# Performance work log

Hardware: AMD Instinct MI355X
Metric: run time of the kernel (lower is better)

## Reference

```python
import jax, jax.numpy as jnp
import numpy as np

# convert_dict = {0: 1, 1: 0, 2: -1}: maps argmax position -> signed label
CONVERT = jnp.array([1, 0, -1], dtype=jnp.int32)


def setup_inputs() -> dict:
    key = jax.random.key(0)
    N = 8388608  # rows; each row is [up(3), none(3), down(3)]
    inputs = jax.random.normal(key, (N, 9), dtype=jnp.float32)
    return {"inputs": inputs}


def reference(inputs):
    # [N, 9] -> [N, 3 groups (up, none, down), 3]
    x = inputs.reshape(-1, 3, 3)

    # __get_max_index: if the max is tied within a 3-vector -> 0,
    # else convert_dict[argmax] in {1, 0, -1}
    maxv = jnp.max(x, axis=-1, keepdims=True)
    ties = jnp.sum((x == maxv).astype(jnp.int32), axis=-1) > 1  # [N, 3]
    mi = jnp.where(ties, 0, CONVERT[jnp.argmax(x, axis=-1)])    # [N, 3] int32

    # calc_value = abs(max_index_none) * (up_idx + none_idx + down_idx)
    calc = jnp.abs(mi[:, 1]) * (mi[:, 0] + mi[:, 1] + mi[:, 2])  # [N] int32

    # __remove_ex_data: keep vector only when sign(calc) matches sign(max_index),
    # otherwise replace by zeros
    c = calc[:, None]
    keep = ((c > 0) & (mi > 0)) | ((c < 0) & (mi < 0)) | ((c == 0) & (mi == 0))
    vecs = jnp.where(keep[..., None], x, jnp.float32(0))  # [N, 3, 3]

    # __concat_result branch: calc==0 -> compare element 1; calc>=1 -> element 0;
    # calc<=-1 -> element 2 (calc is always an integer in {-3..3})
    idx = jnp.where(calc == 0, 1, jnp.where(calc >= 1, 0, 2))  # [N]

    # __find_best_data: argmax over [up[idx], none[idx], down[idx]] picks the
    # winning group (tf.argmax over the concat -> 0=up, 1=none, 2=down, which
    # matches group order here); return that whole (possibly zeroed) 3-vector
    vals = jnp.take_along_axis(vecs, idx[:, None, None], axis=2)[..., 0]  # [N, 3]
    win = jnp.argmax(vals, axis=1)  # [N]
    out = jnp.take_along_axis(vecs, win[:, None, None], axis=1)[:, 0, :]  # [N, 3]
    return out
```

## Files before the change

### kernel.cpp

```cpp
#include <hip/hip_runtime.h>

#define ROWS_PER_BLOCK 256
#define BLOCK_THREADS 256

__global__ __launch_bounds__(BLOCK_THREADS) void pick_rows_kernel(
    const float* __restrict__ in, float* __restrict__ out, long long nrows) {

    __shared__ float lds_in[ROWS_PER_BLOCK * 9];
    __shared__ float lds_out[ROWS_PER_BLOCK * 3];

    const int tid = threadIdx.x;
    const long long tileStride = (long long)gridDim.x * ROWS_PER_BLOCK;

    for (long long rowBase = (long long)blockIdx.x * ROWS_PER_BLOCK;
         rowBase < nrows; rowBase += tileStride) {

        const long long rowsLeft = nrows - rowBase;
        const int rowsHere = rowsLeft < ROWS_PER_BLOCK ? (int)rowsLeft : ROWS_PER_BLOCK;

        const float* src = in + rowBase * 9;
        if (rowsHere == ROWS_PER_BLOCK) {
            const float4* src4 = reinterpret_cast<const float4*>(src);
            #pragma unroll
            for (int i = 0; i < 576 / BLOCK_THREADS + 1; ++i) {
                int k = tid + i * BLOCK_THREADS;
                if (k < 576) {
                    float4 v = src4[k];
                    lds_in[k * 4 + 0] = v.x;
                    lds_in[k * 4 + 1] = v.y;
                    lds_in[k * 4 + 2] = v.z;
                    lds_in[k * 4 + 3] = v.w;
                }
            }
        } else {
            const int nf = rowsHere * 9;
            for (int k = tid; k < nf; k += BLOCK_THREADS) lds_in[k] = src[k];
        }
        __syncthreads();

        if (tid < rowsHere) {
            float v[3][3];
            #pragma unroll
            for (int j = 0; j < 3; ++j)
                #pragma unroll
                for (int k = 0; k < 3; ++k)
                    v[j][k] = lds_in[tid * 9 + j * 3 + k];

            int mi[3];
            #pragma unroll
            for (int j = 0; j < 3; ++j) {
                const float a = v[j][0], b = v[j][1], c = v[j][2];
                const float m = fmaxf(a, fmaxf(b, c));
                const int ties = (int)(a == m) + (int)(b == m) + (int)(c == m);
                int am;
                if (a == m) am = 0;
                else if (b == m) am = 1;
                else am = 2;
                mi[j] = (ties > 1) ? 0 : (1 - am);
            }

            const int calc = (mi[1] < 0 ? -mi[1] : mi[1]) * (mi[0] + mi[1] + mi[2]);

            bool keep[3];
            #pragma unroll
            for (int j = 0; j < 3; ++j)
                keep[j] = (calc > 0 && mi[j] > 0) ||
                          (calc < 0 && mi[j] < 0) ||
                          (calc == 0 && mi[j] == 0);

            const int idx = (calc == 0) ? 1 : ((calc >= 1) ? 0 : 2);

            float vals[3];
            #pragma unroll
            for (int j = 0; j < 3; ++j)
                vals[j] = keep[j] ? v[j][idx] : 0.0f;

            int win = 0;
            float best = vals[0];
            if (vals[1] > best) { best = vals[1]; win = 1; }
            if (vals[2] > best) { win = 2; }

            const bool kw = keep[win];
            #pragma unroll
            for (int k = 0; k < 3; ++k)
                lds_out[tid * 3 + k] = kw ? v[win][k] : 0.0f;
        }
        __syncthreads();

        float* dst = out + rowBase * 3;
        if (rowsHere == ROWS_PER_BLOCK) {
            float4* dst4 = reinterpret_cast<float4*>(dst);
            if (tid < 192) {
                float4 o;
                o.x = lds_out[tid * 4 + 0];
                o.y = lds_out[tid * 4 + 1];
                o.z = lds_out[tid * 4 + 2];
                o.w = lds_out[tid * 4 + 3];
                dst4[tid] = o;
            }
        } else {
            const int nf = rowsHere * 3;
            for (int k = tid; k < nf; k += BLOCK_THREADS) dst[k] = lds_out[k];
        }
        __syncthreads();
    }
}

extern "C" void kernel_launch(void* const* d_in, const int* in_sizes, int n_in,
                              void* d_out, int out_size, void* d_ws, size_t ws_size,
                              hipStream_t stream) {
    const float* in = (const float*)d_in[0];
    float* out = (float*)d_out;
    const long long nrows = (long long)in_sizes[0] / 9;

    const long long tiles = (nrows + ROWS_PER_BLOCK - 1) / ROWS_PER_BLOCK;
    int grid = (int)(tiles < 2048 ? tiles : 2048);
    pick_rows_kernel<<<grid, BLOCK_THREADS, 0, stream>>>(in, out, nrows);
}
```

Baseline: 80.53 us.

## Replace LDS-staged tiles with per-thread 4-row register loads

New measurement: 80.19 us. No clear change (-0.4%).

```diff
diff --git a/kernel.cpp b/kernel.cpp
--- a/kernel.cpp
+++ b/kernel.cpp
@@ -1,108 +1,109 @@
 #include <hip/hip_runtime.h>
 
-#define ROWS_PER_BLOCK 256
-#define BLOCK_THREADS 256
 
-__global__ __launch_bounds__(BLOCK_THREADS) void pick_rows_kernel(
+__device__ __forceinline__ void compute_row(
+    float v00, float v01, float v02,
+    float v10, float v11, float v12,
+    float v20, float v21, float v22,
+    float& o0, float& o1, float& o2) {
+
+    float v[3][3] = {{v00, v01, v02}, {v10, v11, v12}, {v20, v21, v22}};
+
+    int mi[3];
+#pragma unroll
+    for (int j = 0; j < 3; ++j) {
+        const float a = v[j][0], b = v[j][1], c = v[j][2];
+        const float m = fmaxf(a, fmaxf(b, c));
+        const int ties = (int)(a == m) + (int)(b == m) + (int)(c == m);
+        int am;
+        if (a == m) am = 0;
+        else if (b == m) am = 1;
+        else am = 2;
+        mi[j] = (ties > 1) ? 0 : (1 - am);
+    }
+
+    const int calc = (mi[1] < 0 ? -mi[1] : mi[1]) * (mi[0] + mi[1] + mi[2]);
+
+    bool keep[3];
+#pragma unroll
+    for (int j = 0; j < 3; ++j)
+        keep[j] = (calc > 0 && mi[j] > 0) ||
+                  (calc < 0 && mi[j] < 0) ||
+                  (calc == 0 && mi[j] == 0);
+
+    const int idx = (calc == 0) ? 1 : ((calc >= 1) ? 0 : 2);
+
+    float vals[3];
+#pragma unroll
+    for (int j = 0; j < 3; ++j) {
+        const float vj = (idx == 0) ? v[j][0] : ((idx == 2) ? v[j][2] : v[j][1]);
+        vals[j] = keep[j] ? vj : 0.0f;
+    }
+
+    const bool w1 = vals[1] > vals[0];
+    const float b01 = w1 ? vals[1] : vals[0];
+    const bool w2 = vals[2] > b01;
+
+    const bool keepw = w2 ? keep[2] : (w1 ? keep[1] : keep[0]);
+
+    const float r0 = w2 ? v[2][0] : (w1 ? v[1][0] : v[0][0]);
+    const float r1 = w2 ? v[2][1] : (w1 ? v[1][1] : v[0][1]);
+    const float r2 = w2 ? v[2][2] : (w1 ? v[1][2] : v[0][2]);
+
+    o0 = keepw ? r0 : 0.0f;
+    o1 = keepw ? r1 : 0.0f;
+    o2 = keepw ? r2 : 0.0f;
+}
+
+__global__ __launch_bounds__(256) void pick_rows_kernel(
     const float* __restrict__ in, float* __restrict__ out, long long nrows) {
 
-    __shared__ float lds_in[ROWS_PER_BLOCK * 9];
-    __shared__ float lds_out[ROWS_PER_BLOCK * 3];
+    const long long t = (long long)blockIdx.x * blockDim.x + threadIdx.x;
+    const long long r0 = t * 4;
+    if (r0 >= nrows) return;
 
-    const int tid = threadIdx.x;
-    const long long tileStride = (long long)gridDim.x * ROWS_PER_BLOCK;
+    if (r0 + 4 <= nrows) {
+        const float4* p4 = reinterpret_cast<const float4*>(in + r0 * 9);
+        float4 f[9];
+#pragma unroll
+        for (int i = 0; i < 9; ++i) f[i] = p4[i];
 
-    for (long long rowBase = (long long)blockIdx.x * ROWS_PER_BLOCK;
-         rowBase < nrows; rowBase += tileStride) {
+        float x[36];
+#pragma unroll
+        for (int i = 0; i < 9; ++i) {
+            x[i * 4 + 0] = f[i].x;
+            x[i * 4 + 1] = f[i].y;
+            x[i * 4 + 2] = f[i].z;
+            x[i * 4 + 3] = f[i].w;
+        }
 
-        const long long rowsLeft = nrows - rowBase;
-        const int rowsHere = rowsLeft < ROWS_PER_BLOCK ? (int)rowsLeft : ROWS_PER_BLOCK;
+        float o[12];
+#pragma unroll
+        for (int j = 0; j < 4; ++j) {
+            compute_row(x[j * 9 + 0], x[j * 9 + 1], x[j * 9 + 2],
+                        x[j * 9 + 3], x[j * 9 + 4], x[j * 9 + 5],
+                        x[j * 9 + 6], x[j * 9 + 7], x[j * 9 + 8],
+                        o[j * 3 + 0], o[j * 3 + 1], o[j * 3 + 2]);
+        }
 
-        const float* src = in + rowBase * 9;
-        if (rowsHere == ROWS_PER_BLOCK) {
-            const float4* src4 = reinterpret_cast<const float4*>(src);
-            #pragma unroll
-            for (int i = 0; i < 576 / BLOCK_THREADS + 1; ++i) {
-                int k = tid + i * BLOCK_THREADS;
-                if (k < 576) {
-                    float4 v = src4[k];
-                    lds_in[k * 4 + 0] = v.x;
-                    lds_in[k * 4 + 1] = v.y;
-                    lds_in[k * 4 + 2] = v.z;
-                    lds_in[k * 4 + 3] = v.w;
-                }
-            }
-        } else {
-            const int nf = rowsHere * 9;
-            for (int k = tid; k < nf; k += BLOCK_THREADS) lds_in[k] = src[k];
+        float4* q4 = reinterpret_cast<float4*>(out + r0 * 3);
+        float4 q;
+        q.x = o[0];  q.y = o[1];  q.z = o[2];  q.w = o[3];
+        q4[0] = q;
+        q.x = o[4];  q.y = o[5];  q.z = o[6];  q.w = o[7];
+        q4[1] = q;
+        q.x = o[8];  q.y = o[9];  q.z = o[10]; q.w = o[11];
+        q4[2] = q;
+    } else {
+        for (long long r = r0; r < nrows; ++r) {
+            const float* p = in + r * 9;
+            float o0, o1, o2;
+            compute_row(p[0], p[1], p[2], p[3], p[4], p[5], p[6], p[7], p[8],
+                        o0, o1, o2);
+            out[r * 3 + 0] = o0;
+            out[r * 3 + 1] = o1;
+            out[r * 3 + 2] = o2;
         }
-        __syncthreads();
-
-        if (tid < rowsHere) {
-            float v[3][3];
-            #pragma unroll
-            for (int j = 0; j < 3; ++j)
-                #pragma unroll
-                for (int k = 0; k < 3; ++k)
-                    v[j][k] = lds_in[tid * 9 + j * 3 + k];
-
-            int mi[3];
-            #pragma unroll
-            for (int j = 0; j < 3; ++j) {
-                const float a = v[j][0], b = v[j][1], c = v[j][2];
-                const float m = fmaxf(a, fmaxf(b, c));
-                const int ties = (int)(a == m) + (int)(b == m) + (int)(c == m);
-                int am;
-                if (a == m) am = 0;
-                else if (b == m) am = 1;
-                else am = 2;
-                mi[j] = (ties > 1) ? 0 : (1 - am);
-            }
-
-            const int calc = (mi[1] < 0 ? -mi[1] : mi[1]) * (mi[0] + mi[1] + mi[2]);
-
-            bool keep[3];
-            #pragma unroll
-            for (int j = 0; j < 3; ++j)
-                keep[j] = (calc > 0 && mi[j] > 0) ||
-                          (calc < 0 && mi[j] < 0) ||
-                          (calc == 0 && mi[j] == 0);
-
-            const int idx = (calc == 0) ? 1 : ((calc >= 1) ? 0 : 2);
-
-            float vals[3];
-            #pragma unroll
-            for (int j = 0; j < 3; ++j)
-                vals[j] = keep[j] ? v[j][idx] : 0.0f;
-
-            int win = 0;
-            float best = vals[0];
-            if (vals[1] > best) { best = vals[1]; win = 1; }
-            if (vals[2] > best) { win = 2; }
-
-            const bool kw = keep[win];
-            #pragma unroll
-            for (int k = 0; k < 3; ++k)
-                lds_out[tid * 3 + k] = kw ? v[win][k] : 0.0f;
-        }
-        __syncthreads();
-
-        float* dst = out + rowBase * 3;
-        if (rowsHere == ROWS_PER_BLOCK) {
-            float4* dst4 = reinterpret_cast<float4*>(dst);
-            if (tid < 192) {
-                float4 o;
-                o.x = lds_out[tid * 4 + 0];
-                o.y = lds_out[tid * 4 + 1];
-                o.z = lds_out[tid * 4 + 2];
-                o.w = lds_out[tid * 4 + 3];
-                dst4[tid] = o;
-            }
-        } else {
-            const int nf = rowsHere * 3;
-            for (int k = tid; k < nf; k += BLOCK_THREADS) dst[k] = lds_out[k];
-        }
-        __syncthreads();
     }
 }
 
@@ -113,7 +114,8 @@
     float* out = (float*)d_out;
     const long long nrows = (long long)in_sizes[0] / 9;
 
-    const long long tiles = (nrows + ROWS_PER_BLOCK - 1) / ROWS_PER_BLOCK;
-    int grid = (int)(tiles < 2048 ? tiles : 2048);
-    pick_rows_kernel<<<grid, BLOCK_THREADS, 0, stream>>>(in, out, nrows);
+    const long long nthreads = (nrows + 3) / 4;
+    const int block = 256;
+    const long long nblocks = (nthreads + block - 1) / block;
+    pick_rows_kernel<<<(int)nblocks, block, 0, stream>>>(in, out, nrows);
 }
```

## Use nontemporal loads, drop output LDS staging, and make row selection branchless

Applied to the files above, without the earlier changes.

New measurement: 70.26 us. -12.8%, faster.

```diff
diff --git a/kernel.cpp b/kernel.cpp
--- a/kernel.cpp
+++ b/kernel.cpp
@@ -1,13 +1,64 @@
 #include <hip/hip_runtime.h>
+
+typedef float floatx4 __attribute__((ext_vector_type(4)));
 
 #define ROWS_PER_BLOCK 256
 #define BLOCK_THREADS 256
+
+
+__device__ __forceinline__ void compute_row(
+    const float v[3][3], float& o0, float& o1, float& o2) {
+
+    int mi[3];
+#pragma unroll
+    for (int j = 0; j < 3; ++j) {
+        const float a = v[j][0], b = v[j][1], c = v[j][2];
+        const float m = fmaxf(a, fmaxf(b, c));
+        const int ties = (int)(a == m) + (int)(b == m) + (int)(c == m);
+        int am;
+        if (a == m) am = 0;
+        else if (b == m) am = 1;
+        else am = 2;
+        mi[j] = (ties > 1) ? 0 : (1 - am);
+    }
+
+    const int calc = (mi[1] < 0 ? -mi[1] : mi[1]) * (mi[0] + mi[1] + mi[2]);
+
+    bool keep[3];
+#pragma unroll
+    for (int j = 0; j < 3; ++j)
+        keep[j] = (calc > 0 && mi[j] > 0) ||
+                  (calc < 0 && mi[j] < 0) ||
+                  (calc == 0 && mi[j] == 0);
+
+    const int idx = (calc == 0) ? 1 : ((calc >= 1) ? 0 : 2);
+
+    float vals[3];
+#pragma unroll
+    for (int j = 0; j < 3; ++j) {
+        const float vj = (idx == 0) ? v[j][0] : ((idx == 2) ? v[j][2] : v[j][1]);
+        vals[j] = keep[j] ? vj : 0.0f;
+    }
+
+    const bool w1 = vals[1] > vals[0];
+    const float b01 = w1 ? vals[1] : vals[0];
+    const bool w2 = vals[2] > b01;
+
+    const bool keepw = w2 ? keep[2] : (w1 ? keep[1] : keep[0]);
+
+    const float r0 = w2 ? v[2][0] : (w1 ? v[1][0] : v[0][0]);
+    const float r1 = w2 ? v[2][1] : (w1 ? v[1][1] : v[0][1]);
+    const float r2 = w2 ? v[2][2] : (w1 ? v[1][2] : v[0][2]);
+
+    o0 = keepw ? r0 : 0.0f;
+    o1 = keepw ? r1 : 0.0f;
+    o2 = keepw ? r2 : 0.0f;
+}
 
 __global__ __launch_bounds__(BLOCK_THREADS) void pick_rows_kernel(
     const float* __restrict__ in, float* __restrict__ out, long long nrows) {
 
     __shared__ float lds_in[ROWS_PER_BLOCK * 9];
-    __shared__ float lds_out[ROWS_PER_BLOCK * 3];
 
     const int tid = threadIdx.x;
     const long long tileStride = (long long)gridDim.x * ROWS_PER_BLOCK;
@@ -18,21 +69,29 @@
         const long long rowsLeft = nrows - rowBase;
         const int rowsHere = rowsLeft < ROWS_PER_BLOCK ? (int)rowsLeft : ROWS_PER_BLOCK;
 
-        const float* src = in + rowBase * 9;
         if (rowsHere == ROWS_PER_BLOCK) {
-            const float4* src4 = reinterpret_cast<const float4*>(src);
-            #pragma unroll
-            for (int i = 0; i < 576 / BLOCK_THREADS + 1; ++i) {
-                int k = tid + i * BLOCK_THREADS;
-                if (k < 576) {
-                    float4 v = src4[k];
-                    lds_in[k * 4 + 0] = v.x;
-                    lds_in[k * 4 + 1] = v.y;
-                    lds_in[k * 4 + 2] = v.z;
-                    lds_in[k * 4 + 3] = v.w;
+            const floatx4* src4 = reinterpret_cast<const floatx4*>(in + rowBase * 9);
+            {
+                floatx4 v0 = __builtin_nontemporal_load(src4 + tid);
+                floatx4 v1 = __builtin_nontemporal_load(src4 + tid + 256);
+                lds_in[tid * 4 + 0] = v0.x;
+                lds_in[tid * 4 + 1] = v0.y;
+                lds_in[tid * 4 + 2] = v0.z;
+                lds_in[tid * 4 + 3] = v0.w;
+                lds_in[(tid + 256) * 4 + 0] = v1.x;
+                lds_in[(tid + 256) * 4 + 1] = v1.y;
+                lds_in[(tid + 256) * 4 + 2] = v1.z;
+                lds_in[(tid + 256) * 4 + 3] = v1.w;
+                if (tid < 64) {
+                    floatx4 v2 = __builtin_nontemporal_load(src4 + tid + 512);
+                    lds_in[(tid + 512) * 4 + 0] = v2.x;
+                    lds_in[(tid + 512) * 4 + 1] = v2.y;
+                    lds_in[(tid + 512) * 4 + 2] = v2.z;
+                    lds_in[(tid + 512) * 4 + 3] = v2.w;
                 }
             }
         } else {
+            const float* src = in + rowBase * 9;
             const int nf = rowsHere * 9;
             for (int k = tid; k < nf; k += BLOCK_THREADS) lds_in[k] = src[k];
         }
@@ -40,67 +99,19 @@
 
         if (tid < rowsHere) {
             float v[3][3];
-            #pragma unroll
+#pragma unroll
             for (int j = 0; j < 3; ++j)
-                #pragma unroll
+#pragma unroll
                 for (int k = 0; k < 3; ++k)
                     v[j][k] = lds_in[tid * 9 + j * 3 + k];
 
-            int mi[3];
-            #pragma unroll
-            for (int j = 0; j < 3; ++j) {
-                const float a = v[j][0], b = v[j][1], c = v[j][2];
-                const float m = fmaxf(a, fmaxf(b, c));
-                const int ties = (int)(a == m) + (int)(b == m) + (int)(c == m);
-                int am;
-                if (a == m) am = 0;
-                else if (b == m) am = 1;
-                else am = 2;
-                mi[j] = (ties > 1) ? 0 : (1 - am);
-            }
+            float o0, o1, o2;
+            compute_row(v, o0, o1, o2);
 
-            const int calc = (mi[1] < 0 ? -mi[1] : mi[1]) * (mi[0] + mi[1] + mi[2]);
-
-            bool keep[3];
-            #pragma unroll
-            for (int j = 0; j < 3; ++j)
-                keep[j] = (calc > 0 && mi[j] > 0) ||
-                          (calc < 0 && mi[j] < 0) ||
-                          (calc == 0 && mi[j] == 0);
-
-            const int idx = (calc == 0) ? 1 : ((calc >= 1) ? 0 : 2);
-
-            float vals[3];
-            #pragma unroll
-            for (int j = 0; j < 3; ++j)
-                vals[j] = keep[j] ? v[j][idx] : 0.0f;
-
-            int win = 0;
-            float best = vals[0];
-            if (vals[1] > best) { best = vals[1]; win = 1; }
-            if (vals[2] > best) { win = 2; }
-
-            const bool kw = keep[win];
-            #pragma unroll
-            for (int k = 0; k < 3; ++k)
-                lds_out[tid * 3 + k] = kw ? v[win][k] : 0.0f;
-        }
-        __syncthreads();
-
-        float* dst = out + rowBase * 3;
-        if (rowsHere == ROWS_PER_BLOCK) {
-            float4* dst4 = reinterpret_cast<float4*>(dst);
-            if (tid < 192) {
-                float4 o;
-                o.x = lds_out[tid * 4 + 0];
-                o.y = lds_out[tid * 4 + 1];
-                o.z = lds_out[tid * 4 + 2];
-                o.w = lds_out[tid * 4 + 3];
-                dst4[tid] = o;
-            }
-        } else {
-            const int nf = rowsHere * 3;
-            for (int k = tid; k < nf; k += BLOCK_THREADS) dst[k] = lds_out[k];
+            float* dst = out + (rowBase + tid) * 3;
+            dst[0] = o0;
+            dst[1] = o1;
+            dst[2] = o2;
         }
         __syncthreads();
     }
```
